# Kernel optimization log

Hardware: AMD Instinct MI355X
Metric: run time of the kernel (lower is better)

The kernel has to match this reference:

```python
import jax, jax.numpy as jnp
import numpy as np

B, H, D = 4, 16, 64
CTX, BLK = 3072, 1024
ST, HID = 64, 1024
NUM_RELATIONS = 7
KV = CTX + BLK


def setup_inputs() -> dict:
    key = jax.random.key(0)
    ks = jax.random.split(key, 7)
    return {
        "q": jax.random.normal(ks[0], (B, H, BLK, D), jnp.float32),
        "k": jax.random.normal(ks[1], (B, H, KV, D), jnp.float32),
        "v": jax.random.normal(ks[2], (B, H, KV, D), jnp.float32),
        "block_vertex_ids": jax.random.randint(ks[3], (B, BLK), 0, ST, dtype=jnp.int32),
        "vertex_embedding": jax.random.normal(ks[4], (ST, HID), jnp.float32) * 0.02,
        "relation_bias": jax.random.normal(ks[5], (NUM_RELATIONS, H), jnp.float32) * 0.02,
        "relation_matrix": jax.random.randint(ks[6], (ST, ST), 0, NUM_RELATIONS, dtype=jnp.int32),
        "ctx_len": CTX,
        "block_len": BLK,
    }


def reference(q, k, v, block_vertex_ids, vertex_embedding, relation_bias,
              relation_matrix, ctx_len, block_len):
    # q: [B,H,BLK,D]; k,v: [B,H,CTX+BLK,D]
    st = vertex_embedding.shape[0]
    vid = block_vertex_ids % st                      # [B, BLK] (mod st_size, as in score_mod)
    # get_initial_bias: vertex embedding lookup -> [B, BLK, HID]
    init_bias = vertex_embedding[vid]
    # attention scores
    scale = q.shape[-1] ** -0.5
    scores = jnp.einsum('bhqd,bhkd->bhqk', q, k) * scale   # [B,H,BLK,KV]
    # relational bias only for kv_idx >= ctx_len (blk_idx = kv_idx - ctx_len);
    # for kv_idx < ctx_len the score_mod adds zero.
    rel = relation_matrix[vid[:, :, None], vid[:, None, :]]  # [B, BLK, BLK]
    bias = relation_bias[rel]                                # [B, BLK, BLK, H]
    bias = jnp.transpose(bias, (0, 3, 1, 2))                 # [B, H, BLK(q), BLK(k)]
    scores = scores.at[:, :, :, ctx_len:ctx_len + block_len].add(bias)
    attn = jax.nn.softmax(scores, axis=-1)
    out = jnp.einsum('bhqk,bhkd->bhqd', attn, v)             # [B,H,BLK,D]
    return out, init_bias
```

## Files before the change

kernel.cpp:

```cpp
#include <hip/hip_runtime.h>

#define B_    4
#define H_    16
#define D_    64
#define BLK_  1024
#define CTX_  3072
#define KV_   4096
#define ST_   64
#define HID_  1024
#define NREL_ 7
#define NT_   (KV_ / 64)
#define CTXT_ (CTX_ / 64)

#define LOG2E 1.44269504088896340736f

typedef short  bf16x8_t __attribute__((ext_vector_type(8)));
typedef float  f32x4_t  __attribute__((ext_vector_type(4)));
typedef unsigned int u32x4_t __attribute__((ext_vector_type(4)));

typedef unsigned int uint_as1 __attribute__((address_space(1)));
typedef unsigned int uint_as3 __attribute__((address_space(3)));

__device__ inline void gload16(const void* g, void* l) {
    __builtin_amdgcn_global_load_lds((const uint_as1*)g, (uint_as3*)l, 16, 0, 0);
}

__device__ inline unsigned short f2bf(float f) {
    unsigned int u = __float_as_uint(f);
    u = (u + 0x7FFFu + ((u >> 16) & 1u)) >> 16;
    return (unsigned short)u;
}
__device__ inline float bf2f(unsigned short u) {
    return __uint_as_float(((unsigned int)u) << 16);
}
__device__ inline unsigned int cvtpk(float a, float b) {
    unsigned int r;
    asm("v_cvt_pk_bf16_f32 %0, %1, %2" : "=v"(r) : "v"(a), "v"(b));
    return r;
}

__device__ inline int swz(int row, int col) {
    return row * 64 + (col ^ ((row & 7) << 3));
}

__global__ void prep_kv(const float* __restrict__ kg, const float* __restrict__ vg,
                        unsigned short* __restrict__ kimg, unsigned short* __restrict__ vimg)
{
    __shared__ float tile[64][65];
    const int  gb   = blockIdx.x;
    const bool isV  = gb >= (B_ * H_ * NT_);
    const int  blk  = isV ? gb - B_ * H_ * NT_ : gb;
    const float* src = (isV ? vg : kg) + (size_t)blk * 64 * 64;
    unsigned short* dst = (isV ? vimg : kimg) + (size_t)blk * 4096;

    if (!isV) {
        for (int c = threadIdx.x; c < 512; c += 256) {
            const int row = c >> 3, d0 = (c & 7) << 3;
            const f32x4_t a0 = *(const f32x4_t*)(src + row * 64 + d0);
            const f32x4_t a1 = *(const f32x4_t*)(src + row * 64 + d0 + 4);
            u32x4_t o;
            o[0] = cvtpk(a0[0], a0[1]); o[1] = cvtpk(a0[2], a0[3]);
            o[2] = cvtpk(a1[0], a1[1]); o[3] = cvtpk(a1[2], a1[3]);
            *(u32x4_t*)&dst[swz(row, d0)] = o;
        }
    } else {
        for (int c = threadIdx.x; c < 512; c += 256) {
            const int row = c >> 3, d0 = (c & 7) << 3;
            const f32x4_t a0 = *(const f32x4_t*)(src + row * 64 + d0);
            const f32x4_t a1 = *(const f32x4_t*)(src + row * 64 + d0 + 4);
#pragma unroll
            for (int j = 0; j < 4; ++j) { tile[row][d0 + j] = a0[j]; tile[row][d0 + 4 + j] = a1[j]; }
        }
        __syncthreads();
        for (int c = threadIdx.x; c < 512; c += 256) {
            const int d = c >> 3, k0 = (c & 7) << 3;
            u32x4_t o;
#pragma unroll
            for (int j = 0; j < 4; ++j)
                o[j] = cvtpk(tile[k0 + 2 * j][d], tile[k0 + 2 * j + 1][d]);
            *(u32x4_t*)&dst[swz(d, k0)] = o;
        }
    }
}

__global__ __launch_bounds__(256, 2)
void attn_v5(const float* __restrict__ qg,
             const unsigned short* __restrict__ kimg,
             const unsigned short* __restrict__ vimg,
             const int* __restrict__ bvi,
             const float* __restrict__ rbias, const int* __restrict__ rmat,
             float* __restrict__ outg)
{
    __shared__ __align__(16) unsigned short Kb [2][64 * 64];
    __shared__ __align__(16) unsigned short Vtb[2][64 * 64];
    __shared__ __align__(16) unsigned short Pt[4 * 2 * 16 * 64];
    __shared__ unsigned short btab[64 * 64];
    __shared__ unsigned char  vkl8[BLK_];

    const int tid  = threadIdx.x;
    const int w    = tid >> 6;
    const int lane = tid & 63;
    const int lo   = lane & 15;
    const int hi   = lane >> 4;

    const int bid  = blockIdx.x;
    const int xcd  = bid & 7;
    const int slot = bid >> 3;
    const int bh   = (slot >> 3) * 8 + xcd;
    const int qt   = slot & 7;
    const int b    = bh >> 4;
    const int h    = bh & 15;
    const int q0   = qt * 128;

    for (int i = tid; i < 64 * 64; i += 256)
        btab[i] = f2bf(rbias[rmat[i] * H_ + h] * LOG2E);
    for (int i = tid; i < BLK_; i += 256)
        vkl8[i] = (unsigned char)(bvi[b * BLK_ + i] & (ST_ - 1));

    bf16x8_t qa[2][2];
    int viq[2][4];
#pragma unroll
    for (int sub = 0; sub < 2; ++sub) {
        const int row0 = q0 + w * 32 + sub * 16;
        const float* qrow = qg + ((size_t)bh * BLK_ + row0 + lo) * D_;
#pragma unroll
        for (int kk = 0; kk < 2; ++kk) {
            const f32x4_t x0 = *(const f32x4_t*)(qrow + kk * 32 + hi * 8);
            const f32x4_t x1 = *(const f32x4_t*)(qrow + kk * 32 + hi * 8 + 4);
#pragma unroll
            for (int j = 0; j < 4; ++j) {
                qa[sub][kk][j]     = (short)f2bf(x0[j] * (0.125f * LOG2E));
                qa[sub][kk][4 + j] = (short)f2bf(x1[j] * (0.125f * LOG2E));
            }
        }
#pragma unroll
        for (int r = 0; r < 4; ++r)
            viq[sub][r] = bvi[b * BLK_ + row0 + hi * 4 + r] & (ST_ - 1);
    }

    f32x4_t oacc[2][4];
#pragma unroll
    for (int sub = 0; sub < 2; ++sub)
#pragma unroll
        for (int blk = 0; blk < 4; ++blk) oacc[sub][blk] = (f32x4_t){0.f, 0.f, 0.f, 0.f};
    float lrow[2][4] = {{0.f, 0.f, 0.f, 0.f}, {0.f, 0.f, 0.f, 0.f}};

    const char* kbase = (const char*)(kimg + (size_t)bh * NT_ * 4096);
    const char* vbase = (const char*)(vimg + (size_t)bh * NT_ * 4096);

    auto stage = [&](unsigned short* Kl, unsigned short* Vl, int t) {
        const char* kg16 = kbase + (size_t)t * 8192 + w * 2048 + lane * 16;
        const char* vg16 = vbase + (size_t)t * 8192 + w * 2048 + lane * 16;
        char* kl = (char*)Kl + w * 2048;
        char* vl = (char*)Vl + w * 2048;
        gload16(kg16,        kl);
        gload16(kg16 + 1024, kl + 1024);
        gload16(vg16,        vl);
        gload16(vg16 + 1024, vl + 1024);
    };

    auto compute = [&](const unsigned short* Kl, const unsigned short* Vl, int t) {
        f32x4_t sacc[2][4];
#pragma unroll
        for (int sub = 0; sub < 2; ++sub)
#pragma unroll
            for (int blk = 0; blk < 4; ++blk) sacc[sub][blk] = (f32x4_t){0.f, 0.f, 0.f, 0.f};
#pragma unroll
        for (int kk = 0; kk < 2; ++kk) {
#pragma unroll
            for (int blk = 0; blk < 4; ++blk) {
                const bf16x8_t kb = *(const bf16x8_t*)&Kl[swz(blk * 16 + lo, kk * 32 + hi * 8)];
                sacc[0][blk] = __builtin_amdgcn_mfma_f32_16x16x32_bf16(qa[0][kk], kb, sacc[0][blk], 0, 0, 0);
                sacc[1][blk] = __builtin_amdgcn_mfma_f32_16x16x32_bf16(qa[1][kk], kb, sacc[1][blk], 0, 0, 0);
            }
        }
        if (t >= CTXT_) {
            const int base = (t - CTXT_) * 64;
#pragma unroll
            for (int blk = 0; blk < 4; ++blk) {
                const int vj = vkl8[base + blk * 16 + lo];
#pragma unroll
                for (int sub = 0; sub < 2; ++sub)
#pragma unroll
                    for (int r = 0; r < 4; ++r)
                        sacc[sub][blk][r] += bf2f(btab[viq[sub][r] * 64 + vj]);
            }
        }
#pragma unroll
        for (int sub = 0; sub < 2; ++sub) {
            unsigned short* pw = &Pt[w * 2048 + sub * 1024];
#pragma unroll
            for (int blk = 0; blk < 4; ++blk) {
#pragma unroll
                for (int r = 0; r < 4; ++r) {
                    const float p = exp2f(sacc[sub][blk][r]);
                    sacc[sub][blk][r] = p;
                    lrow[sub][r] += p;
                }
                const int col = blk * 16 + lo;
                const unsigned int p01 = cvtpk(sacc[sub][blk][0], sacc[sub][blk][1]);
                const unsigned int p23 = cvtpk(sacc[sub][blk][2], sacc[sub][blk][3]);
                pw[swz(hi * 4 + 0, col)] = (unsigned short)p01;
                pw[swz(hi * 4 + 1, col)] = (unsigned short)(p01 >> 16);
                pw[swz(hi * 4 + 2, col)] = (unsigned short)p23;
                pw[swz(hi * 4 + 3, col)] = (unsigned short)(p23 >> 16);
            }
        }
#pragma unroll
        for (int kk = 0; kk < 2; ++kk) {
            const bf16x8_t pa0 = *(const bf16x8_t*)&Pt[w * 2048 +        swz(lo, kk * 32 + hi * 8)];
            const bf16x8_t pa1 = *(const bf16x8_t*)&Pt[w * 2048 + 1024 + swz(lo, kk * 32 + hi * 8)];
#pragma unroll
            for (int blk = 0; blk < 4; ++blk) {
                const bf16x8_t vb = *(const bf16x8_t*)&Vl[swz(blk * 16 + lo, kk * 32 + hi * 8)];
                oacc[0][blk] = __builtin_amdgcn_mfma_f32_16x16x32_bf16(pa0, vb, oacc[0][blk], 0, 0, 0);
                oacc[1][blk] = __builtin_amdgcn_mfma_f32_16x16x32_bf16(pa1, vb, oacc[1][blk], 0, 0, 0);
            }
        }
    };

    stage(Kb[0], Vtb[0], 0);
    __syncthreads();

    for (int i = 0; i < NT_ / 2; ++i) {
        const int t0 = 2 * i, t1 = 2 * i + 1;
        stage(Kb[1], Vtb[1], t1);
        compute(Kb[0], Vtb[0], t0);
        __syncthreads();
        if (t1 + 1 < NT_) stage(Kb[0], Vtb[0], t1 + 1);
        compute(Kb[1], Vtb[1], t1);
        __syncthreads();
    }

#pragma unroll
    for (int sub = 0; sub < 2; ++sub) {
#pragma unroll
        for (int off = 1; off < 16; off <<= 1) {
#pragma unroll
            for (int r = 0; r < 4; ++r) lrow[sub][r] += __shfl_xor(lrow[sub][r], off, 64);
        }
        float inv[4];
#pragma unroll
        for (int r = 0; r < 4; ++r) inv[r] = 1.0f / lrow[sub][r];
        float* ob = outg + ((size_t)bh * BLK_ + q0 + w * 32 + sub * 16) * D_;
#pragma unroll
        for (int blk = 0; blk < 4; ++blk) {
#pragma unroll
            for (int r = 0; r < 4; ++r)
                ob[(hi * 4 + r) * D_ + blk * 16 + lo] = oacc[sub][blk][r] * inv[r];
        }
    }
}

__global__ __launch_bounds__(256, 3)
void attn_v1(const float* __restrict__ qg, const float* __restrict__ kg,
             const float* __restrict__ vg, const int* __restrict__ bvi,
             const float* __restrict__ rbias, const int* __restrict__ rmat,
             float* __restrict__ outg)
{
    __shared__ __align__(16) unsigned short Kt[64 * 64];
    __shared__ __align__(16) unsigned short Vs[64 * 64];
    __shared__ __align__(16) unsigned short Vt[64 * 64];
    __shared__ __align__(16) unsigned short Pt[4 * 16 * 64];
    __shared__ float btab[64 * 64];
    __shared__ int   vkl[64];

    const int tid  = threadIdx.x;
    const int w    = tid >> 6;
    const int lane = tid & 63;
    const int lo   = lane & 15;
    const int hi   = lane >> 4;

    const int bid  = blockIdx.x;
    const int xcd  = bid & 7;
    const int slot = bid >> 3;
    const int bh   = (slot >> 4) * 8 + xcd;
    const int qt   = slot & 15;
    const int b    = bh >> 4;
    const int h    = bh & 15;
    const int q0   = qt * 64;

    for (int i = tid; i < 64 * 64; i += 256)
        btab[i] = rbias[rmat[i] * H_ + h];

    const float* qrow = qg + ((size_t)bh * BLK_ + q0 + w * 16 + lo) * D_;
    bf16x8_t qa[2];
#pragma unroll
    for (int kk = 0; kk < 2; ++kk) {
        const f32x4_t x0 = *(const f32x4_t*)(qrow + kk * 32 + hi * 8);
        const f32x4_t x1 = *(const f32x4_t*)(qrow + kk * 32 + hi * 8 + 4);
#pragma unroll
        for (int j = 0; j < 4; ++j) {
            qa[kk][j]     = (short)f2bf(x0[j] * 0.125f);
            qa[kk][4 + j] = (short)f2bf(x1[j] * 0.125f);
        }
    }

    int viq[4];
#pragma unroll
    for (int r = 0; r < 4; ++r)
        viq[r] = bvi[b * BLK_ + q0 + w * 16 + hi * 4 + r] & (ST_ - 1);

    f32x4_t oacc[4];
#pragma unroll
    for (int blk = 0; blk < 4; ++blk) oacc[blk] = (f32x4_t){0.f, 0.f, 0.f, 0.f};
    float mrow[4], lrow[4];
#pragma unroll
    for (int r = 0; r < 4; ++r) { mrow[r] = -INFINITY; lrow[r] = 0.f; }

    const size_t kvbase = (size_t)bh * KV_ * D_;

    for (int t = 0; t < NT_; ++t) {
        const int kv0 = t * 64;
        __syncthreads();
#pragma unroll
        for (int c = tid; c < 512; c += 256) {
            const int row = c >> 3, d0 = (c & 7) << 3;
            const float* ksrc = kg + kvbase + (size_t)(kv0 + row) * D_ + d0;
            const float* vsrc = vg + kvbase + (size_t)(kv0 + row) * D_ + d0;
            const f32x4_t a0 = *(const f32x4_t*)ksrc, a1 = *(const f32x4_t*)(ksrc + 4);
            const f32x4_t b0 = *(const f32x4_t*)vsrc, b1 = *(const f32x4_t*)(vsrc + 4);
            bf16x8_t kv8, vv8;
#pragma unroll
            for (int j = 0; j < 4; ++j) {
                kv8[j]     = (short)f2bf(a0[j]); kv8[4 + j] = (short)f2bf(a1[j]);
                vv8[j]     = (short)f2bf(b0[j]); vv8[4 + j] = (short)f2bf(b1[j]);
            }
            *(bf16x8_t*)&Kt[swz(row, d0)] = kv8;
            *(bf16x8_t*)&Vs[swz(row, d0)] = vv8;
        }
        const bool isb = (kv0 >= CTX_);
        if (isb && tid < 64) vkl[tid] = bvi[b * BLK_ + (kv0 - CTX_) + tid] & (ST_ - 1);
        __syncthreads();

#pragma unroll
        for (int c = tid; c < 512; c += 256) {
            const int dcol = c >> 3, kvc = (c & 7) << 3;
            bf16x8_t tv;
#pragma unroll
            for (int j = 0; j < 8; ++j) tv[j] = (short)Vs[swz(kvc + j, dcol)];
            *(bf16x8_t*)&Vt[swz(dcol, kvc)] = tv;
        }

        f32x4_t sacc[4];
#pragma unroll
        for (int blk = 0; blk < 4; ++blk) sacc[blk] = (f32x4_t){0.f, 0.f, 0.f, 0.f};
#pragma unroll
        for (int kk = 0; kk < 2; ++kk) {
#pragma unroll
            for (int blk = 0; blk < 4; ++blk) {
                const bf16x8_t kb = *(const bf16x8_t*)&Kt[swz(blk * 16 + lo, kk * 32 + hi * 8)];
                sacc[blk] = __builtin_amdgcn_mfma_f32_16x16x32_bf16(qa[kk], kb, sacc[blk], 0, 0, 0);
            }
        }
        if (isb) {
#pragma unroll
            for (int blk = 0; blk < 4; ++blk) {
                const int vj = vkl[blk * 16 + lo];
#pragma unroll
                for (int r = 0; r < 4; ++r) sacc[blk][r] += btab[viq[r] * 64 + vj];
            }
        }
        f32x4_t tm = sacc[0];
#pragma unroll
        for (int blk = 1; blk < 4; ++blk)
#pragma unroll
            for (int r = 0; r < 4; ++r) tm[r] = fmaxf(tm[r], sacc[blk][r]);
#pragma unroll
        for (int off = 1; off < 16; off <<= 1) {
#pragma unroll
            for (int r = 0; r < 4; ++r) tm[r] = fmaxf(tm[r], __shfl_xor(tm[r], off, 64));
        }
        float corr[4];
#pragma unroll
        for (int r = 0; r < 4; ++r) {
            const float mn = fmaxf(mrow[r], tm[r]);
            corr[r] = __expf(mrow[r] - mn);
            mrow[r] = mn;
        }
        f32x4_t psum = (f32x4_t){0.f, 0.f, 0.f, 0.f};
#pragma unroll
        for (int blk = 0; blk < 4; ++blk) {
#pragma unroll
            for (int r = 0; r < 4; ++r) {
                const float p = __expf(sacc[blk][r] - mrow[r]);
                sacc[blk][r] = p;
                psum[r] += p;
            }
        }
#pragma unroll
        for (int off = 1; off < 16; off <<= 1) {
#pragma unroll
            for (int r = 0; r < 4; ++r) psum[r] += __shfl_xor(psum[r], off, 64);
        }
#pragma unroll
        for (int r = 0; r < 4; ++r) lrow[r] = lrow[r] * corr[r] + psum[r];
#pragma unroll
        for (int blk = 0; blk < 4; ++blk)
#pragma unroll
            for (int r = 0; r < 4; ++r) oacc[blk][r] *= corr[r];

        unsigned short* pw = &Pt[w * 1024];
#pragma unroll
        for (int blk = 0; blk < 4; ++blk) {
            const int col = blk * 16 + lo;
#pragma unroll
            for (int r = 0; r < 4; ++r)
                pw[swz(hi * 4 + r, col)] = f2bf(sacc[blk][r]);
        }
        __syncthreads();
#pragma unroll
        for (int kk = 0; kk < 2; ++kk) {
            const bf16x8_t pa = *(const bf16x8_t*)&Pt[w * 1024 + swz(lo, kk * 32 + hi * 8)];
#pragma unroll
            for (int blk = 0; blk < 4; ++blk) {
                const bf16x8_t vb = *(const bf16x8_t*)&Vt[swz(blk * 16 + lo, kk * 32 + hi * 8)];
                oacc[blk] = __builtin_amdgcn_mfma_f32_16x16x32_bf16(pa, vb, oacc[blk], 0, 0, 0);
            }
        }
    }

    float* ob = outg + ((size_t)bh * BLK_ + q0 + w * 16) * D_;
#pragma unroll
    for (int blk = 0; blk < 4; ++blk) {
#pragma unroll
        for (int r = 0; r < 4; ++r)
            ob[(hi * 4 + r) * D_ + blk * 16 + lo] = oacc[blk][r] / lrow[r];
    }
}

__global__ void ibias_kernel(const int* __restrict__ bvi,
                             const float* __restrict__ emb,
                             float* __restrict__ out2)
{
    const int bq  = blockIdx.x;
    const int vid = bvi[bq] & (ST_ - 1);
    const f32x4_t* src = (const f32x4_t*)(emb + (size_t)vid * HID_);
    f32x4_t*       dst = (f32x4_t*)(out2 + (size_t)bq * HID_);
    for (int i = threadIdx.x; i < HID_ / 4; i += 256) dst[i] = src[i];
}

extern "C" void kernel_launch(void* const* d_in, const int* in_sizes, int n_in,
                              void* d_out, int out_size, void* d_ws, size_t ws_size,
                              hipStream_t stream)
{
    const float* qg    = (const float*)d_in[0];
    const float* kg    = (const float*)d_in[1];
    const float* vg    = (const float*)d_in[2];
    const int*   bvi   = (const int*)d_in[3];
    const float* emb   = (const float*)d_in[4];
    const float* rbias = (const float*)d_in[5];
    const int*   rmat  = (const int*)d_in[6];

    float* outg = (float*)d_out;
    float* out2 = outg + (size_t)B_ * H_ * BLK_ * D_;

    const size_t img_elems = (size_t)B_ * H_ * KV_ * D_;
    const size_t need      = 2 * img_elems * sizeof(unsigned short);

    if (ws_size >= need) {
        unsigned short* kimg = (unsigned short*)d_ws;
        unsigned short* vimg = kimg + img_elems;
        prep_kv<<<dim3(2 * B_ * H_ * NT_), dim3(256), 0, stream>>>(kg, vg, kimg, vimg);
        attn_v5<<<dim3(B_ * H_ * (BLK_ / 128)), dim3(256), 0, stream>>>(
            qg, kimg, vimg, bvi, rbias, rmat, outg);
    } else {
        attn_v1<<<dim3(B_ * H_ * (BLK_ / 64)), dim3(256), 0, stream>>>(
            qg, kg, vg, bvi, rbias, rmat, outg);
    }
    ibias_kernel<<<dim3(B_ * BLK_), dim3(256), 0, stream>>>(bvi, emb, out2);
}
```

Before: 315.2 us.

## Compute softmax row sums via MFMA, halve P scratch, raise occupancy

The row sum of exponentials is now accumulated by extra MFMAs against a vector of bf16 ones instead of scalar adds plus a cross-lane shuffle reduction at the end. The P tile in shared memory is halved by processing the two 16-row subtiles one after another. V fragments are loaded into registers once and reused for both subtiles. Launch bounds move from 2 to 3 blocks per CU to raise occupancy. The trade-offs are more MFMA work per tile, bf16 rounding in the denominator that now matches the numerator, and register pressure that could cause spills.

```diff
diff --git a/kernel.cpp b/kernel.cpp
--- a/kernel.cpp
+++ b/kernel.cpp
@@ -83,8 +83,8 @@
     }
 }
 
-__global__ __launch_bounds__(256, 2)
-void attn_v5(const float* __restrict__ qg,
+__global__ __launch_bounds__(256, 3)
+void attn_v6(const float* __restrict__ qg,
              const unsigned short* __restrict__ kimg,
              const unsigned short* __restrict__ vimg,
              const int* __restrict__ bvi,
@@ -93,7 +93,7 @@
 {
     __shared__ __align__(16) unsigned short Kb [2][64 * 64];
     __shared__ __align__(16) unsigned short Vtb[2][64 * 64];
-    __shared__ __align__(16) unsigned short Pt[4 * 2 * 16 * 64];
+    __shared__ __align__(16) unsigned short Pt[4 * 16 * 64];
     __shared__ unsigned short btab[64 * 64];
     __shared__ unsigned char  vkl8[BLK_];
 
@@ -138,12 +138,16 @@
             viq[sub][r] = bvi[b * BLK_ + row0 + hi * 4 + r] & (ST_ - 1);
     }
 
+    bf16x8_t ones;
+#pragma unroll
+    for (int j = 0; j < 8; ++j) ones[j] = (short)0x3F80;
+
     f32x4_t oacc[2][4];
 #pragma unroll
     for (int sub = 0; sub < 2; ++sub)
 #pragma unroll
         for (int blk = 0; blk < 4; ++blk) oacc[sub][blk] = (f32x4_t){0.f, 0.f, 0.f, 0.f};
-    float lrow[2][4] = {{0.f, 0.f, 0.f, 0.f}, {0.f, 0.f, 0.f, 0.f}};
+    f32x4_t lacc[2] = {(f32x4_t){0.f, 0.f, 0.f, 0.f}, (f32x4_t){0.f, 0.f, 0.f, 0.f}};
 
     const char* kbase = (const char*)(kimg + (size_t)bh * NT_ * 4096);
     const char* vbase = (const char*)(vimg + (size_t)bh * NT_ * 4096);
@@ -186,17 +190,21 @@
                         sacc[sub][blk][r] += bf2f(btab[viq[sub][r] * 64 + vj]);
             }
         }
+        bf16x8_t vbr[2][4];
+#pragma unroll
+        for (int kk = 0; kk < 2; ++kk)
+#pragma unroll
+            for (int blk = 0; blk < 4; ++blk)
+                vbr[kk][blk] = *(const bf16x8_t*)&Vl[swz(blk * 16 + lo, kk * 32 + hi * 8)];
+
+        unsigned short* pw = &Pt[w * 1024];
 #pragma unroll
         for (int sub = 0; sub < 2; ++sub) {
-            unsigned short* pw = &Pt[w * 2048 + sub * 1024];
-#pragma unroll
-            for (int blk = 0; blk < 4; ++blk) {
-#pragma unroll
-                for (int r = 0; r < 4; ++r) {
-                    const float p = exp2f(sacc[sub][blk][r]);
-                    sacc[sub][blk][r] = p;
-                    lrow[sub][r] += p;
-                }
+#pragma unroll
+            for (int blk = 0; blk < 4; ++blk) {
+#pragma unroll
+                for (int r = 0; r < 4; ++r)
+                    sacc[sub][blk][r] = exp2f(sacc[sub][blk][r]);
                 const int col = blk * 16 + lo;
                 const unsigned int p01 = cvtpk(sacc[sub][blk][0], sacc[sub][blk][1]);
                 const unsigned int p23 = cvtpk(sacc[sub][blk][2], sacc[sub][blk][3]);
@@ -205,17 +213,15 @@
                 pw[swz(hi * 4 + 2, col)] = (unsigned short)p23;
                 pw[swz(hi * 4 + 3, col)] = (unsigned short)(p23 >> 16);
             }
-        }
-#pragma unroll
-        for (int kk = 0; kk < 2; ++kk) {
-            const bf16x8_t pa0 = *(const bf16x8_t*)&Pt[w * 2048 +        swz(lo, kk * 32 + hi * 8)];
-            const bf16x8_t pa1 = *(const bf16x8_t*)&Pt[w * 2048 + 1024 + swz(lo, kk * 32 + hi * 8)];
-#pragma unroll
-            for (int blk = 0; blk < 4; ++blk) {
-                const bf16x8_t vb = *(const bf16x8_t*)&Vl[swz(blk * 16 + lo, kk * 32 + hi * 8)];
-                oacc[0][blk] = __builtin_amdgcn_mfma_f32_16x16x32_bf16(pa0, vb, oacc[0][blk], 0, 0, 0);
-                oacc[1][blk] = __builtin_amdgcn_mfma_f32_16x16x32_bf16(pa1, vb, oacc[1][blk], 0, 0, 0);
-            }
+            const bf16x8_t pa0 = *(const bf16x8_t*)&Pt[w * 1024 + swz(lo, 0 * 32 + hi * 8)];
+            const bf16x8_t pa1 = *(const bf16x8_t*)&Pt[w * 1024 + swz(lo, 1 * 32 + hi * 8)];
+#pragma unroll
+            for (int blk = 0; blk < 4; ++blk) {
+                oacc[sub][blk] = __builtin_amdgcn_mfma_f32_16x16x32_bf16(pa0, vbr[0][blk], oacc[sub][blk], 0, 0, 0);
+                oacc[sub][blk] = __builtin_amdgcn_mfma_f32_16x16x32_bf16(pa1, vbr[1][blk], oacc[sub][blk], 0, 0, 0);
+            }
+            lacc[sub] = __builtin_amdgcn_mfma_f32_16x16x32_bf16(pa0, ones, lacc[sub], 0, 0, 0);
+            lacc[sub] = __builtin_amdgcn_mfma_f32_16x16x32_bf16(pa1, ones, lacc[sub], 0, 0, 0);
         }
     };
 
@@ -234,14 +240,9 @@
 
 #pragma unroll
     for (int sub = 0; sub < 2; ++sub) {
-#pragma unroll
-        for (int off = 1; off < 16; off <<= 1) {
-#pragma unroll
-            for (int r = 0; r < 4; ++r) lrow[sub][r] += __shfl_xor(lrow[sub][r], off, 64);
-        }
         float inv[4];
 #pragma unroll
-        for (int r = 0; r < 4; ++r) inv[r] = 1.0f / lrow[sub][r];
+        for (int r = 0; r < 4; ++r) inv[r] = 1.0f / lacc[sub][r];
         float* ob = outg + ((size_t)bh * BLK_ + q0 + w * 32 + sub * 16) * D_;
 #pragma unroll
         for (int blk = 0; blk < 4; ++blk) {
@@ -462,7 +463,7 @@
         unsigned short* kimg = (unsigned short*)d_ws;
         unsigned short* vimg = kimg + img_elems;
         prep_kv<<<dim3(2 * B_ * H_ * NT_), dim3(256), 0, stream>>>(kg, vg, kimg, vimg);
-        attn_v5<<<dim3(B_ * H_ * (BLK_ / 128)), dim3(256), 0, stream>>>(
+        attn_v6<<<dim3(B_ * H_ * (BLK_ / 128)), dim3(256), 0, stream>>>(
             qg, kimg, vimg, bvi, rbias, rmat, outg);
     } else {
         attn_v1<<<dim3(B_ * H_ * (BLK_ / 64)), dim3(256), 0, stream>>>(
```

Result: faster. 308.0 us (-2.3%).
